# Kernel optimization log

Measured on AMD Instinct MI355X. Metric: run time of the kernel, lower is better.

The kernel has to match this reference:

```python
import jax, jax.numpy as jnp
import numpy as np

EPS = 1e-5

def _layernorm(x, gamma, beta):
    mu = jnp.mean(x, axis=-1, keepdims=True)
    var = jnp.var(x, axis=-1, keepdims=True)
    return (x - mu) * jax.lax.rsqrt(var + EPS) * gamma + beta

def setup_inputs() -> dict:
    key = jax.random.key(0)
    ks = jax.random.split(key, 8)
    B, I, H = 8192, 1024, 1024
    s_w = 1.0 / np.sqrt(I)
    s_u = 1.0 / np.sqrt(H)
    return {
        "x": jax.random.normal(ks[0], (B, I), jnp.float32),
        "h": jax.random.normal(ks[1], (B, H), jnp.float32),
        "c": jax.random.normal(ks[2], (B, H), jnp.float32),
        "W_w": jax.random.uniform(ks[3], (I, 4 * H), jnp.float32, -s_w, s_w),
        "W_b": jax.random.uniform(ks[4], (4 * H,), jnp.float32, -s_w, s_w),
        "U_w": jax.random.uniform(ks[5], (H, 4 * H), jnp.float32, -s_u, s_u),
        "ln_g_gamma": jnp.ones((4 * H,), jnp.float32),
        "ln_g_beta": jnp.zeros((4 * H,), jnp.float32),
        "ln_c_gamma": jnp.ones((H,), jnp.float32),
        "ln_c_beta": jnp.zeros((H,), jnp.float32),
    }

def reference(x, h, c, W_w, W_b, U_w, ln_g_gamma, ln_g_beta, ln_c_gamma, ln_c_beta):
    gates_x = x @ W_w + W_b            # [B, 4H]
    gates_h = h @ U_w                  # [B, 4H]
    gates = gates_x + gates_h + gates_x * gates_h  # multiplicative integration
    gates = _layernorm(gates, ln_g_gamma, ln_g_beta)
    i, f, g, o = jnp.split(gates, 4, axis=-1)
    i = jax.nn.sigmoid(i)
    f = jax.nn.sigmoid(f)
    o = jax.nn.sigmoid(o)
    g = jnp.tanh(g)
    c_new = f * c + i * g
    c_new = _layernorm(c_new, ln_c_gamma, ln_c_beta)
    h_new = o * jnp.tanh(c_new)
    return (h_new, h_new, c_new)
```

## Files before the change

kernel.cpp:

```cpp
#include <hip/hip_runtime.h>
#include <cstdint>


#define MB (1024ull * 1024ull)

typedef short bf16x8 __attribute__((ext_vector_type(8)));
typedef float f32x4  __attribute__((ext_vector_type(4)));

__device__ __forceinline__ bool bf16_mode(const void* g1) {
    return ((const unsigned short*)g1)[0] == 0x3F80u;
}
__device__ __forceinline__ float b2f(unsigned short u) {
    union { unsigned int i; float f; } v; v.i = ((unsigned int)u) << 16; return v.f;
}
__device__ __forceinline__ unsigned short f2b(float f) {
    unsigned int i = __float_as_uint(f);
    unsigned int r = (i + 0x7FFFu + ((i >> 16) & 1u)) >> 16;
    return (unsigned short)r;
}
__device__ __forceinline__ void up4(uint2 v, float* o) {
    o[0] = __uint_as_float(v.x << 16);
    o[1] = __uint_as_float(v.x & 0xFFFF0000u);
    o[2] = __uint_as_float(v.y << 16);
    o[3] = __uint_as_float(v.y & 0xFFFF0000u);
}
__device__ __forceinline__ unsigned int pack2(unsigned short a, unsigned short b) {
    return (unsigned int)a | ((unsigned int)b << 16);
}
__device__ __forceinline__ void ld4(const void* p, size_t idx, bool isbf, float* o) {
    if (isbf) {
        up4(*(const uint2*)((const unsigned short*)p + idx), o);
    } else {
        float4 v = *(const float4*)((const float*)p + idx);
        o[0] = v.x; o[1] = v.y; o[2] = v.z; o[3] = v.w;
    }
}

__device__ __forceinline__ void load_lds16(const unsigned short* g, unsigned short* l) {
    __builtin_amdgcn_global_load_lds(
        (const __attribute__((address_space(1))) unsigned int*)g,
        (__attribute__((address_space(3))) unsigned int*)l,
        16, 0, 0);
}

__global__ __launch_bounds__(256)
void prep_weights(const void* __restrict__ src, const void* __restrict__ g1,
                  unsigned short* __restrict__ dst)
{
    const bool isbf = bf16_mode(g1);
    __shared__ unsigned short tile[64][68];
    const int t  = threadIdx.x;
    const int tx = t & 15;
    const int ty = t >> 4;
    const int bx = blockIdx.x * 64;
    const int by = blockIdx.y * 64;
    if (isbf) {
        const unsigned short* s = (const unsigned short*)src;
#pragma unroll
        for (int it = 0; it < 4; ++it) {
            const int r = ty + it * 16;
            uint2 v = *(const uint2*)(s + (size_t)(by + r) * 4096 + bx + tx * 4);
            tile[r][tx * 4 + 0] = (unsigned short)(v.x & 0xFFFFu);
            tile[r][tx * 4 + 1] = (unsigned short)(v.x >> 16);
            tile[r][tx * 4 + 2] = (unsigned short)(v.y & 0xFFFFu);
            tile[r][tx * 4 + 3] = (unsigned short)(v.y >> 16);
        }
    } else {
        const float* s = (const float*)src;
#pragma unroll
        for (int it = 0; it < 4; ++it) {
            const int r = ty + it * 16;
            float4 v = *(const float4*)(s + (size_t)(by + r) * 4096 + bx + tx * 4);
            tile[r][tx * 4 + 0] = f2b(v.x);
            tile[r][tx * 4 + 1] = f2b(v.y);
            tile[r][tx * 4 + 2] = f2b(v.z);
            tile[r][tx * 4 + 3] = f2b(v.w);
        }
    }
    __syncthreads();
#pragma unroll
    for (int it = 0; it < 4; ++it) {
        const int rn = ty + it * 16;
        const int ck = tx * 4;
        uint2 w;
        w.x = pack2(tile[ck + 0][rn], tile[ck + 1][rn]);
        w.y = pack2(tile[ck + 2][rn], tile[ck + 3][rn]);
        *(uint2*)(dst + (size_t)(bx + rn) * 1024 + by + ck) = w;
    }
}

__global__ __launch_bounds__(256)
void prep_xh(const void* __restrict__ X, const void* __restrict__ Hs,
             const void* __restrict__ g1, void* __restrict__ outb)
{
    if (bf16_mode(g1)) return;
    const float* src = (blockIdx.y == 0) ? (const float*)X : (const float*)Hs;
    unsigned short* dst = (unsigned short*)((char*)outb + (blockIdx.y == 0 ? 48 * MB : 80 * MB));
    const size_t i0 = ((size_t)blockIdx.x * 256 + threadIdx.x) * 8;
    float4 a = *(const float4*)(src + i0);
    float4 b = *(const float4*)(src + i0 + 4);
    uint4 o;
    o.x = pack2(f2b(a.x), f2b(a.y));
    o.y = pack2(f2b(a.z), f2b(a.w));
    o.z = pack2(f2b(b.x), f2b(b.y));
    o.w = pack2(f2b(b.z), f2b(b.w));
    *(uint4*)(dst + i0) = o;
}

#define TM 128
#define TN 128
#define TK 32

__global__ __launch_bounds__(256, 2)
void milstm_gemm(const void* __restrict__ Xraw, const void* __restrict__ Hraw,
                 const void* __restrict__ g1, const void* __restrict__ Wbraw,
                 const void* __restrict__ outb,
                 const unsigned short* __restrict__ Wt,
                 const unsigned short* __restrict__ Ut,
                 unsigned short* __restrict__ G, int m0)
{
    const bool isbf = bf16_mode(g1);
    const unsigned short* X  = isbf ? (const unsigned short*)Xraw
                                    : (const unsigned short*)((const char*)outb + 48 * MB);
    const unsigned short* Hs = isbf ? (const unsigned short*)Hraw
                                    : (const unsigned short*)((const char*)outb + 80 * MB);

    __shared__ __align__(16) unsigned short sAx[TM * TK];
    __shared__ __align__(16) unsigned short sAh[TM * TK];
    __shared__ __align__(16) unsigned short sBw[TN * TK];
    __shared__ __align__(16) unsigned short sBu[TN * TK];

    const int tid  = threadIdx.x;
    const int wave = tid >> 6;
    const int lane = tid & 63;
    const int quad = lane >> 4;
    const int l16  = lane & 15;

    const int bm = blockIdx.y * TM;
    const int bn = blockIdx.x * TN;

    const int wm = (wave & 1) * 64;
    const int wn = (wave >> 1) * 64;

    const int c0   = wave * 2;
    const int srow = lane >> 2;
    const int scol = (lane & 3) * 8;

    const unsigned short* px0 = X  + (size_t)(m0 + bm + (c0 + 0) * 16 + srow) * 1024 + scol;
    const unsigned short* px1 = X  + (size_t)(m0 + bm + (c0 + 1) * 16 + srow) * 1024 + scol;
    const unsigned short* ph0 = Hs + (size_t)(m0 + bm + (c0 + 0) * 16 + srow) * 1024 + scol;
    const unsigned short* ph1 = Hs + (size_t)(m0 + bm + (c0 + 1) * 16 + srow) * 1024 + scol;
    const unsigned short* pw0 = Wt + (size_t)(bn + (c0 + 0) * 16 + srow) * 1024 + scol;
    const unsigned short* pw1 = Wt + (size_t)(bn + (c0 + 1) * 16 + srow) * 1024 + scol;
    const unsigned short* pu0 = Ut + (size_t)(bn + (c0 + 0) * 16 + srow) * 1024 + scol;
    const unsigned short* pu1 = Ut + (size_t)(bn + (c0 + 1) * 16 + srow) * 1024 + scol;

    unsigned short* dax0 = sAx + (c0 + 0) * 16 * TK;
    unsigned short* dax1 = sAx + (c0 + 1) * 16 * TK;
    unsigned short* dah0 = sAh + (c0 + 0) * 16 * TK;
    unsigned short* dah1 = sAh + (c0 + 1) * 16 * TK;
    unsigned short* dbw0 = sBw + (c0 + 0) * 16 * TK;
    unsigned short* dbw1 = sBw + (c0 + 1) * 16 * TK;
    unsigned short* dbu0 = sBu + (c0 + 0) * 16 * TK;
    unsigned short* dbu1 = sBu + (c0 + 1) * 16 * TK;

    f32x4 accx[4][4] = {};
    f32x4 acch[4][4] = {};

    for (int k0 = 0; k0 < 1024; k0 += TK) {
        load_lds16(px0 + k0, dax0);
        load_lds16(px1 + k0, dax1);
        load_lds16(ph0 + k0, dah0);
        load_lds16(ph1 + k0, dah1);
        load_lds16(pw0 + k0, dbw0);
        load_lds16(pw1 + k0, dbw1);
        load_lds16(pu0 + k0, dbu0);
        load_lds16(pu1 + k0, dbu1);
        __syncthreads();

        bf16x8 ax[4], ah[4];
#pragma unroll
        for (int mi = 0; mi < 4; ++mi) {
            ax[mi] = *(const bf16x8*)(sAx + (wm + mi * 16 + l16) * TK + quad * 8);
            ah[mi] = *(const bf16x8*)(sAh + (wm + mi * 16 + l16) * TK + quad * 8);
        }
#pragma unroll
        for (int ni = 0; ni < 4; ++ni) {
            bf16x8 bw = *(const bf16x8*)(sBw + (wn + ni * 16 + l16) * TK + quad * 8);
            bf16x8 bu = *(const bf16x8*)(sBu + (wn + ni * 16 + l16) * TK + quad * 8);
#pragma unroll
            for (int mi = 0; mi < 4; ++mi) {
                accx[mi][ni] = __builtin_amdgcn_mfma_f32_16x16x32_bf16(ax[mi], bw, accx[mi][ni], 0, 0, 0);
                acch[mi][ni] = __builtin_amdgcn_mfma_f32_16x16x32_bf16(ah[mi], bu, acch[mi][ni], 0, 0, 0);
            }
        }
        __syncthreads();
    }

#pragma unroll
    for (int ni = 0; ni < 4; ++ni) {
        const int col = bn + wn + ni * 16 + l16;
        const float bias = isbf ? b2f(((const unsigned short*)Wbraw)[col])
                                : ((const float*)Wbraw)[col];
#pragma unroll
        for (int mi = 0; mi < 4; ++mi) {
            const int row0 = bm + wm + mi * 16 + quad * 4;
#pragma unroll
            for (int r = 0; r < 4; ++r) {
                float gx = accx[mi][ni][r] + bias;
                float gh = acch[mi][ni][r];
                float gv = gx + gh + gx * gh;
                G[(size_t)(row0 + r) * 4096 + col] = f2b(gv);
            }
        }
    }
}

__global__ __launch_bounds__(256)
void milstm_cell(const unsigned short* __restrict__ G,
                 const void* __restrict__ C,
                 const void* __restrict__ g1, const void* __restrict__ b1,
                 const void* __restrict__ g2, const void* __restrict__ b2,
                 void* __restrict__ outb, int m0)
{
    const bool isbf = bf16_mode(g1);
    const int lrow = blockIdx.x;
    const int row  = m0 + lrow;
    const int tid  = threadIdx.x;
    const int lane = tid & 63;
    const int wave = tid >> 6;
    const unsigned short* grow = G + (size_t)lrow * 4096;

    __shared__ float red[16];

    float s = 0.f, ss = 0.f;
    const uint4* gv4 = (const uint4*)grow;
#pragma unroll
    for (int u = 0; u < 2; ++u) {
        uint4 v = gv4[tid * 2 + u];
        unsigned int w[4] = { v.x, v.y, v.z, v.w };
#pragma unroll
        for (int q = 0; q < 4; ++q) {
            float flo = __uint_as_float(w[q] << 16);
            float fhi = __uint_as_float(w[q] & 0xFFFF0000u);
            s  += flo + fhi;
            ss += flo * flo + fhi * fhi;
        }
    }
#pragma unroll
    for (int off = 32; off > 0; off >>= 1) {
        s  += __shfl_xor(s, off, 64);
        ss += __shfl_xor(ss, off, 64);
    }
    if (lane == 0) { red[wave] = s; red[8 + wave] = ss; }
    __syncthreads();
    s  = red[0] + red[1] + red[2] + red[3];
    ss = red[8] + red[9] + red[10] + red[11];
    const float mu   = s * (1.f / 4096.f);
    const float rstd = rsqrtf(fmaxf(ss * (1.f / 4096.f) - mu * mu, 0.f) + 1e-5f);

    const int j0 = tid * 4;
    float xi[4], xf[4], xg[4], xo[4], cc[4];
    float G1[4], B1[4], ii[4], cn[4], ov[4];

    up4(*(const uint2*)(grow + j0),        xi);
    up4(*(const uint2*)(grow + 1024 + j0), xf);
    up4(*(const uint2*)(grow + 2048 + j0), xg);
    up4(*(const uint2*)(grow + 3072 + j0), xo);
    ld4(C, (size_t)row * 1024 + j0, isbf, cc);

    ld4(g1, j0, isbf, G1); ld4(b1, j0, isbf, B1);
#pragma unroll
    for (int q = 0; q < 4; ++q) {
        float z = (xi[q] - mu) * rstd * G1[q] + B1[q];
        ii[q] = 1.f / (1.f + __expf(-z));
    }
    ld4(g1, 1024 + j0, isbf, G1); ld4(b1, 1024 + j0, isbf, B1);
#pragma unroll
    for (int q = 0; q < 4; ++q) {
        float z = (xf[q] - mu) * rstd * G1[q] + B1[q];
        xf[q] = 1.f / (1.f + __expf(-z));
    }
    ld4(g1, 2048 + j0, isbf, G1); ld4(b1, 2048 + j0, isbf, B1);
#pragma unroll
    for (int q = 0; q < 4; ++q) {
        float z = (xg[q] - mu) * rstd * G1[q] + B1[q];
        xg[q] = tanhf(z);
    }
    ld4(g1, 3072 + j0, isbf, G1); ld4(b1, 3072 + j0, isbf, B1);
#pragma unroll
    for (int q = 0; q < 4; ++q) {
        float z = (xo[q] - mu) * rstd * G1[q] + B1[q];
        ov[q] = 1.f / (1.f + __expf(-z));
    }
#pragma unroll
    for (int q = 0; q < 4; ++q) cn[q] = xf[q] * cc[q] + ii[q] * xg[q];

    float s2  = cn[0] + cn[1] + cn[2] + cn[3];
    float ss2 = cn[0]*cn[0] + cn[1]*cn[1] + cn[2]*cn[2] + cn[3]*cn[3];
#pragma unroll
    for (int off = 32; off > 0; off >>= 1) {
        s2  += __shfl_xor(s2, off, 64);
        ss2 += __shfl_xor(ss2, off, 64);
    }
    if (lane == 0) { red[4 + wave] = s2; red[12 + wave] = ss2; }
    __syncthreads();
    s2  = red[4]  + red[5]  + red[6]  + red[7];
    ss2 = red[12] + red[13] + red[14] + red[15];
    const float mu2   = s2 * (1.f / 1024.f);
    const float rstd2 = rsqrtf(fmaxf(ss2 * (1.f / 1024.f) - mu2 * mu2, 0.f) + 1e-5f);

    ld4(g2, j0, isbf, G1);
    ld4(b2, j0, isbf, B1);

    float hv[4], cv[4];
#pragma unroll
    for (int q = 0; q < 4; ++q) {
        cv[q] = (cn[q] - mu2) * rstd2 * G1[q] + B1[q];
        hv[q] = ov[q] * tanhf(cv[q]);
    }

    const size_t BH = (size_t)8192 * 1024;
    if (isbf) {
        unsigned short* out = (unsigned short*)outb;
        uint2 hb, cb;
        hb.x = pack2(f2b(hv[0]), f2b(hv[1])); hb.y = pack2(f2b(hv[2]), f2b(hv[3]));
        cb.x = pack2(f2b(cv[0]), f2b(cv[1])); cb.y = pack2(f2b(cv[2]), f2b(cv[3]));
        *(uint2*)(out + (size_t)row * 1024 + j0)          = hb;
        *(uint2*)(out + BH + (size_t)row * 1024 + j0)     = hb;
        *(uint2*)(out + 2 * BH + (size_t)row * 1024 + j0) = cb;
    } else {
        float* out = (float*)outb;
        float4 hf = { hv[0], hv[1], hv[2], hv[3] };
        float4 cf = { cv[0], cv[1], cv[2], cv[3] };
        *(float4*)(out + (size_t)row * 1024 + j0)          = hf;
        *(float4*)(out + BH + (size_t)row * 1024 + j0)     = hf;
        *(float4*)(out + 2 * BH + (size_t)row * 1024 + j0) = cf;
    }
}

extern "C" void kernel_launch(void* const* d_in, const int* in_sizes, int n_in,
                              void* d_out, int out_size, void* d_ws, size_t ws_size,
                              hipStream_t stream)
{
    const void* X  = d_in[0];
    const void* Hh = d_in[1];
    const void* C  = d_in[2];
    const void* Ww = d_in[3];
    const void* Wb = d_in[4];
    const void* Uw = d_in[5];
    const void* g1 = d_in[6];
    const void* b1 = d_in[7];
    const void* g2 = d_in[8];
    const void* b2 = d_in[9];

    unsigned short* G  = (unsigned short*)d_ws;
    unsigned short* Wt = (unsigned short*)((char*)d_ws + 32 * MB);
    unsigned short* Ut = (unsigned short*)((char*)d_ws + 40 * MB);

    prep_weights<<<dim3(64, 16), 256, 0, stream>>>(Ww, g1, Wt);
    prep_weights<<<dim3(64, 16), 256, 0, stream>>>(Uw, g1, Ut);
    prep_xh<<<dim3(4096, 2), 256, 0, stream>>>(X, Hh, g1, d_out);

    for (int ph = 0; ph < 2; ++ph) {
        const int m0 = ph * 4096;
        milstm_gemm<<<dim3(32, 32), 256, 0, stream>>>(X, Hh, g1, Wb, d_out, Wt, Ut, G, m0);
        milstm_cell<<<dim3(4096), 256, 0, stream>>>(G, C, g1, b1, g2, b2, d_out, m0);
    }
}
```

Baseline: 426.1 us.

## Swizzle GEMM LDS layout, stage gate row in LDS, fast tanh, single-pass launch

```diff
diff --git a/kernel.cpp b/kernel.cpp
--- a/kernel.cpp
+++ b/kernel.cpp
@@ -28,13 +28,11 @@
     return (unsigned int)a | ((unsigned int)b << 16);
 }
 __device__ __forceinline__ void ld4(const void* p, size_t idx, bool isbf, float* o) {
-    if (isbf) {
-        up4(*(const uint2*)((const unsigned short*)p + idx), o);
-    } else {
-        float4 v = *(const float4*)((const float*)p + idx);
-        o[0] = v.x; o[1] = v.y; o[2] = v.z; o[3] = v.w;
-    }
-}
+    if (isbf) up4(*(const uint2*)((const unsigned short*)p + idx), o);
+    else { float4 v = *(const float4*)((const float*)p + idx); o[0]=v.x; o[1]=v.y; o[2]=v.z; o[3]=v.w; }
+}
+__device__ __forceinline__ float fast_sigmoid(float z) { return 1.f / (1.f + __expf(-z)); }
+__device__ __forceinline__ float fast_tanh(float z)    { return 1.f - 2.f / (__expf(2.f * z) + 1.f); }
 
 __device__ __forceinline__ void load_lds16(const unsigned short* g, unsigned short* l) {
     __builtin_amdgcn_global_load_lds(
@@ -144,7 +142,8 @@
 
     const int c0   = wave * 2;
     const int srow = lane >> 2;
-    const int scol = (lane & 3) * 8;
+    const int skb  = (lane & 3) ^ ((srow >> 1) & 3);
+    const int scol = skb * 8;
 
     const unsigned short* px0 = X  + (size_t)(m0 + bm + (c0 + 0) * 16 + srow) * 1024 + scol;
     const unsigned short* px1 = X  + (size_t)(m0 + bm + (c0 + 1) * 16 + srow) * 1024 + scol;
@@ -155,14 +154,16 @@
     const unsigned short* pu0 = Ut + (size_t)(bn + (c0 + 0) * 16 + srow) * 1024 + scol;
     const unsigned short* pu1 = Ut + (size_t)(bn + (c0 + 1) * 16 + srow) * 1024 + scol;
 
-    unsigned short* dax0 = sAx + (c0 + 0) * 16 * TK;
-    unsigned short* dax1 = sAx + (c0 + 1) * 16 * TK;
-    unsigned short* dah0 = sAh + (c0 + 0) * 16 * TK;
-    unsigned short* dah1 = sAh + (c0 + 1) * 16 * TK;
-    unsigned short* dbw0 = sBw + (c0 + 0) * 16 * TK;
-    unsigned short* dbw1 = sBw + (c0 + 1) * 16 * TK;
-    unsigned short* dbu0 = sBu + (c0 + 0) * 16 * TK;
-    unsigned short* dbu1 = sBu + (c0 + 1) * 16 * TK;
+    unsigned short* dax0 = sAx + (c0 + 0) * 512;
+    unsigned short* dax1 = sAx + (c0 + 1) * 512;
+    unsigned short* dah0 = sAh + (c0 + 0) * 512;
+    unsigned short* dah1 = sAh + (c0 + 1) * 512;
+    unsigned short* dbw0 = sBw + (c0 + 0) * 512;
+    unsigned short* dbw1 = sBw + (c0 + 1) * 512;
+    unsigned short* dbu0 = sBu + (c0 + 0) * 512;
+    unsigned short* dbu1 = sBu + (c0 + 1) * 512;
+
+    const int kread = (quad ^ ((l16 >> 1) & 3)) * 8;
 
     f32x4 accx[4][4] = {};
     f32x4 acch[4][4] = {};
@@ -181,13 +182,13 @@
         bf16x8 ax[4], ah[4];
 #pragma unroll
         for (int mi = 0; mi < 4; ++mi) {
-            ax[mi] = *(const bf16x8*)(sAx + (wm + mi * 16 + l16) * TK + quad * 8);
-            ah[mi] = *(const bf16x8*)(sAh + (wm + mi * 16 + l16) * TK + quad * 8);
+            ax[mi] = *(const bf16x8*)(sAx + (wm + mi * 16 + l16) * TK + kread);
+            ah[mi] = *(const bf16x8*)(sAh + (wm + mi * 16 + l16) * TK + kread);
         }
 #pragma unroll
         for (int ni = 0; ni < 4; ++ni) {
-            bf16x8 bw = *(const bf16x8*)(sBw + (wn + ni * 16 + l16) * TK + quad * 8);
-            bf16x8 bu = *(const bf16x8*)(sBu + (wn + ni * 16 + l16) * TK + quad * 8);
+            bf16x8 bw = *(const bf16x8*)(sBw + (wn + ni * 16 + l16) * TK + kread);
+            bf16x8 bu = *(const bf16x8*)(sBu + (wn + ni * 16 + l16) * TK + kread);
 #pragma unroll
             for (int mi = 0; mi < 4; ++mi) {
                 accx[mi][ni] = __builtin_amdgcn_mfma_f32_16x16x32_bf16(ax[mi], bw, accx[mi][ni], 0, 0, 0);
@@ -231,6 +232,7 @@
     const int wave = tid >> 6;
     const unsigned short* grow = G + (size_t)lrow * 4096;
 
+    __shared__ __align__(16) unsigned short srow[4096];
     __shared__ float red[16];
 
     float s = 0.f, ss = 0.f;
@@ -238,6 +240,7 @@
 #pragma unroll
     for (int u = 0; u < 2; ++u) {
         uint4 v = gv4[tid * 2 + u];
+        *(uint4*)(srow + (size_t)(tid * 2 + u) * 8) = v;
         unsigned int w[4] = { v.x, v.y, v.z, v.w };
 #pragma unroll
         for (int q = 0; q < 4; ++q) {
@@ -263,36 +266,24 @@
     float xi[4], xf[4], xg[4], xo[4], cc[4];
     float G1[4], B1[4], ii[4], cn[4], ov[4];
 
-    up4(*(const uint2*)(grow + j0),        xi);
-    up4(*(const uint2*)(grow + 1024 + j0), xf);
-    up4(*(const uint2*)(grow + 2048 + j0), xg);
-    up4(*(const uint2*)(grow + 3072 + j0), xo);
+    up4(*(const uint2*)(srow + j0),        xi);
+    up4(*(const uint2*)(srow + 1024 + j0), xf);
+    up4(*(const uint2*)(srow + 2048 + j0), xg);
+    up4(*(const uint2*)(srow + 3072 + j0), xo);
     ld4(C, (size_t)row * 1024 + j0, isbf, cc);
 
     ld4(g1, j0, isbf, G1); ld4(b1, j0, isbf, B1);
 #pragma unroll
-    for (int q = 0; q < 4; ++q) {
-        float z = (xi[q] - mu) * rstd * G1[q] + B1[q];
-        ii[q] = 1.f / (1.f + __expf(-z));
-    }
+    for (int q = 0; q < 4; ++q) ii[q] = fast_sigmoid((xi[q] - mu) * rstd * G1[q] + B1[q]);
     ld4(g1, 1024 + j0, isbf, G1); ld4(b1, 1024 + j0, isbf, B1);
 #pragma unroll
-    for (int q = 0; q < 4; ++q) {
-        float z = (xf[q] - mu) * rstd * G1[q] + B1[q];
-        xf[q] = 1.f / (1.f + __expf(-z));
-    }
+    for (int q = 0; q < 4; ++q) xf[q] = fast_sigmoid((xf[q] - mu) * rstd * G1[q] + B1[q]);
     ld4(g1, 2048 + j0, isbf, G1); ld4(b1, 2048 + j0, isbf, B1);
 #pragma unroll
-    for (int q = 0; q < 4; ++q) {
-        float z = (xg[q] - mu) * rstd * G1[q] + B1[q];
-        xg[q] = tanhf(z);
-    }
+    for (int q = 0; q < 4; ++q) xg[q] = fast_tanh((xg[q] - mu) * rstd * G1[q] + B1[q]);
     ld4(g1, 3072 + j0, isbf, G1); ld4(b1, 3072 + j0, isbf, B1);
 #pragma unroll
-    for (int q = 0; q < 4; ++q) {
-        float z = (xo[q] - mu) * rstd * G1[q] + B1[q];
-        ov[q] = 1.f / (1.f + __expf(-z));
-    }
+    for (int q = 0; q < 4; ++q) ov[q] = fast_sigmoid((xo[q] - mu) * rstd * G1[q] + B1[q]);
 #pragma unroll
     for (int q = 0; q < 4; ++q) cn[q] = xf[q] * cc[q] + ii[q] * xg[q];
 
@@ -317,7 +308,7 @@
 #pragma unroll
     for (int q = 0; q < 4; ++q) {
         cv[q] = (cn[q] - mu2) * rstd2 * G1[q] + B1[q];
-        hv[q] = ov[q] * tanhf(cv[q]);
+        hv[q] = ov[q] * fast_tanh(cv[q]);
     }
 
     const size_t BH = (size_t)8192 * 1024;
@@ -354,17 +345,24 @@
     const void* g2 = d_in[8];
     const void* b2 = d_in[9];
 
+    const bool single = ws_size >= 80 * MB;
+    const size_t goff = single ? 64 * MB : 32 * MB;
     unsigned short* G  = (unsigned short*)d_ws;
-    unsigned short* Wt = (unsigned short*)((char*)d_ws + 32 * MB);
-    unsigned short* Ut = (unsigned short*)((char*)d_ws + 40 * MB);
+    unsigned short* Wt = (unsigned short*)((char*)d_ws + goff);
+    unsigned short* Ut = (unsigned short*)((char*)d_ws + goff + 8 * MB);
 
     prep_weights<<<dim3(64, 16), 256, 0, stream>>>(Ww, g1, Wt);
     prep_weights<<<dim3(64, 16), 256, 0, stream>>>(Uw, g1, Ut);
     prep_xh<<<dim3(4096, 2), 256, 0, stream>>>(X, Hh, g1, d_out);
 
-    for (int ph = 0; ph < 2; ++ph) {
-        const int m0 = ph * 4096;
-        milstm_gemm<<<dim3(32, 32), 256, 0, stream>>>(X, Hh, g1, Wb, d_out, Wt, Ut, G, m0);
-        milstm_cell<<<dim3(4096), 256, 0, stream>>>(G, C, g1, b1, g2, b2, d_out, m0);
-    }
-}
+    if (single) {
+        milstm_gemm<<<dim3(32, 64), 256, 0, stream>>>(X, Hh, g1, Wb, d_out, Wt, Ut, G, 0);
+        milstm_cell<<<dim3(8192), 256, 0, stream>>>(G, C, g1, b1, g2, b2, d_out, 0);
+    } else {
+        for (int ph = 0; ph < 2; ++ph) {
+            const int m0 = ph * 4096;
+            milstm_gemm<<<dim3(32, 32), 256, 0, stream>>>(X, Hh, g1, Wb, d_out, Wt, Ut, G, m0);
+            milstm_cell<<<dim3(4096), 256, 0, stream>>>(G, C, g1, b1, g2, b2, d_out, m0);
+        }
+    }
+}
```

Result: faster. 399.7 us (-6.2%).
